# Optimization experiments

Hardware: AMD Instinct MI355X
Metric: run time of the kernel (lower is better)

Reference implementation:

```python
import jax, jax.numpy as jnp
import numpy as np

B, LAT, FRAME, HID, E, GH = 4096, 64, 512, 1024, 8, 128
IN1 = LAT + FRAME      # 576, fc1/gate input
IN2 = LAT + HID        # 1088, fc2/fc3 input
OUT = FRAME            # 512, num_future_frames * frame_size


def setup_inputs() -> dict:
    key = jax.random.key(0)
    ks = jax.random.split(key, 16)
    s = lambda fan_in: 1.0 / np.sqrt(fan_in)
    inp = {
        "z": jax.random.normal(ks[0], (B, LAT), jnp.float32),
        "c": jax.random.normal(ks[1], (B, FRAME), jnp.float32),
        # expert-mixed layers: weight [E, in, out], bias [E, out]
        "w0": jax.random.uniform(ks[2], (E, IN1, HID), jnp.float32, -s(IN1), s(IN1)),
        "b0": jax.random.uniform(ks[3], (E, HID), jnp.float32, -s(IN1), s(IN1)),
        "w1": jax.random.uniform(ks[4], (E, IN2, HID), jnp.float32, -s(IN2), s(IN2)),
        "b1": jax.random.uniform(ks[5], (E, HID), jnp.float32, -s(IN2), s(IN2)),
        "w2": jax.random.uniform(ks[6], (E, IN2, OUT), jnp.float32, -s(IN2), s(IN2)),
        "b2": jax.random.uniform(ks[7], (E, OUT), jnp.float32, -s(IN2), s(IN2)),
        # gate MLP
        "gw1": jax.random.uniform(ks[8], (IN1, GH), jnp.float32, -s(IN1), s(IN1)),
        "gb1": jax.random.uniform(ks[9], (GH,), jnp.float32, -s(IN1), s(IN1)),
        "gw2": jax.random.uniform(ks[10], (GH, GH), jnp.float32, -s(GH), s(GH)),
        "gb2": jax.random.uniform(ks[11], (GH,), jnp.float32, -s(GH), s(GH)),
        "gw3": jax.random.uniform(ks[12], (GH, E), jnp.float32, -s(GH), s(GH)),
        "gb3": jax.random.uniform(ks[13], (E,), jnp.float32, -s(GH), s(GH)),
    }
    return inp


def _mixed_layer(coef, x, w, b):
    # per-expert projection then softmax-weighted mix: same math as
    # baddbmm(coef@b, x, (coef@flat(w)).view(B,in,out)) in the original.
    ye = jnp.einsum('bi,eio->beo', x, w)          # [B, E, out]
    return jnp.einsum('be,beo->bo', coef, ye) + coef @ b


def reference(z, c, w0, b0, w1, b1, w2, b2, gw1, gb1, gw2, gb2, gw3, gb3):
    x0 = jnp.concatenate([z, c], axis=1)           # [B, IN1]
    h = jax.nn.elu(x0 @ gw1 + gb1)
    h = jax.nn.elu(h @ gw2 + gb2)
    coef = jax.nn.softmax(h @ gw3 + gb3, axis=1)   # [B, E]

    out = jax.nn.elu(_mixed_layer(coef, x0, w0, b0))
    out = jax.nn.elu(_mixed_layer(coef, jnp.concatenate([z, out], axis=1), w1, b1))
    out = _mixed_layer(coef, jnp.concatenate([z, out], axis=1), w2, b2)
    return out
```

## Files before the change

kernel.cpp:

```cpp
#include <hip/hip_runtime.h>
#include <cstdint>
#include <cstddef>

#define B_    4096
#define LAT   64
#define FRAME 512
#define HID   1024
#define NE    8
#define GH    128
#define IN1   576
#define IN2   1088

typedef _Float16 half8 __attribute__((ext_vector_type(8)));
typedef float  f32x4  __attribute__((ext_vector_type(4)));

__device__ inline void async16(const void* g, void* l) {
  __builtin_amdgcn_global_load_lds(
      (__attribute__((address_space(1))) void*)(void*)g,
      (__attribute__((address_space(3))) void*)l, 16, 0, 0);
}

__device__ inline float elu(float v) { return v > 0.f ? v : expm1f(v); }

__global__ __launch_bounds__(256) void prep_gatew(
    const float* __restrict__ gw1, const float* __restrict__ gw2,
    _Float16* __restrict__ gw1T, _Float16* __restrict__ gw2T)
{
  __shared__ float t[32][33];
  const int tx = threadIdx.x, ty = threadIdx.y;
  int bx = blockIdx.x;
  const float* in; _Float16* out; int K, N, kt, nt;
  if (bx < 72) { in = gw1; out = gw1T; K = 576; N = 128; kt = bx >> 2; nt = bx & 3; }
  else { bx -= 72; in = gw2; out = gw2T; K = 128; N = 128; kt = bx >> 2; nt = bx & 3; }
  const int k0 = kt * 32, n0 = nt * 32;
  for (int it = 0; it < 4; ++it)
    t[ty + it * 8][tx] = in[(size_t)(k0 + ty + it * 8) * N + n0 + tx];
  __syncthreads();
  for (int it = 0; it < 4; ++it)
    out[(size_t)(n0 + ty + it * 8) * K + k0 + tx] = (_Float16)t[tx][ty + it * 8];
}

__global__ __launch_bounds__(256) void gate_mfma(
    const float* __restrict__ z, const float* __restrict__ c,
    const _Float16* __restrict__ gw1T,
    const _Float16* __restrict__ gw2T,
    const float* __restrict__ gb1, const float* __restrict__ gb2,
    const float* __restrict__ gw3, const float* __restrict__ gb3,
    float* __restrict__ coef)
{
  __shared__ _Float16 h_lds[128][136];
  __shared__ float    h2_lds[128][129];
  __shared__ float    gw3s[128 * 8];
  const int tid = threadIdx.x;
  const int wave = tid >> 6, lane = tid & 63;
  const int quad = lane >> 4, l16 = lane & 15;
  const int r0 = blockIdx.x * 128;

  for (int i = tid; i < 128 * 8; i += 256) gw3s[i] = gw3[i];

  f32x4 acc[2][8];
  #pragma unroll
  for (int mt = 0; mt < 2; ++mt)
    #pragma unroll
    for (int nt = 0; nt < 8; ++nt)
      #pragma unroll
      for (int r = 0; r < 4; ++r) acc[mt][nt][r] = 0.f;

  #pragma unroll 2
  for (int s = 0; s < 18; ++s) {
    const int k0 = s * 32;
    half8 af[2];
    #pragma unroll
    for (int mt = 0; mt < 2; ++mt) {
      const size_t row = r0 + wave * 32 + mt * 16 + l16;
      const float* src = (k0 < LAT) ? z + row * LAT + k0 + quad * 8
                                    : c + row * FRAME + (k0 - LAT) + quad * 8;
      f32x4 lo = *(const f32x4*)src, hi = *(const f32x4*)(src + 4);
      #pragma unroll
      for (int j = 0; j < 4; ++j) { af[mt][j] = (_Float16)lo[j]; af[mt][j + 4] = (_Float16)hi[j]; }
    }
    half8 bfr[8];
    #pragma unroll
    for (int nt = 0; nt < 8; ++nt)
      bfr[nt] = *(const half8*)(gw1T + (size_t)(nt * 16 + l16) * 576 + k0 + quad * 8);
    #pragma unroll
    for (int mt = 0; mt < 2; ++mt)
      #pragma unroll
      for (int nt = 0; nt < 8; ++nt)
        acc[mt][nt] = __builtin_amdgcn_mfma_f32_16x16x32_f16(af[mt], bfr[nt], acc[mt][nt], 0, 0, 0);
  }
  #pragma unroll
  for (int mt = 0; mt < 2; ++mt)
    #pragma unroll
    for (int nt = 0; nt < 8; ++nt)
      #pragma unroll
      for (int r = 0; r < 4; ++r) {
        const int rowl = wave * 32 + mt * 16 + quad * 4 + r;
        const int col = nt * 16 + l16;
        h_lds[rowl][col] = (_Float16)elu(acc[mt][nt][r] + gb1[col]);
      }
  __syncthreads();

  f32x4 acc2[2][8];
  #pragma unroll
  for (int mt = 0; mt < 2; ++mt)
    #pragma unroll
    for (int nt = 0; nt < 8; ++nt)
      #pragma unroll
      for (int r = 0; r < 4; ++r) acc2[mt][nt][r] = 0.f;
  #pragma unroll
  for (int s = 0; s < 4; ++s) {
    const int k0 = s * 32;
    half8 af[2];
    #pragma unroll
    for (int mt = 0; mt < 2; ++mt)
      af[mt] = *(const half8*)&h_lds[wave * 32 + mt * 16 + l16][k0 + quad * 8];
    half8 bfr[8];
    #pragma unroll
    for (int nt = 0; nt < 8; ++nt)
      bfr[nt] = *(const half8*)(gw2T + (size_t)(nt * 16 + l16) * 128 + k0 + quad * 8);
    #pragma unroll
    for (int mt = 0; mt < 2; ++mt)
      #pragma unroll
      for (int nt = 0; nt < 8; ++nt)
        acc2[mt][nt] = __builtin_amdgcn_mfma_f32_16x16x32_f16(af[mt], bfr[nt], acc2[mt][nt], 0, 0, 0);
  }
  #pragma unroll
  for (int mt = 0; mt < 2; ++mt)
    #pragma unroll
    for (int nt = 0; nt < 8; ++nt)
      #pragma unroll
      for (int r = 0; r < 4; ++r) {
        const int rowl = wave * 32 + mt * 16 + quad * 4 + r;
        const int col = nt * 16 + l16;
        h2_lds[rowl][col] = elu(acc2[mt][nt][r] + gb2[col]);
      }
  __syncthreads();

  {
    const int row = tid >> 1, eh = (tid & 1) * 4;
    float l4[4];
    #pragma unroll
    for (int j = 0; j < 4; ++j) l4[j] = gb3[eh + j];
    for (int k = 0; k < 128; ++k) {
      const float hv = h2_lds[row][k];
      #pragma unroll
      for (int j = 0; j < 4; ++j) l4[j] += hv * gw3s[k * 8 + eh + j];
    }
    float m4 = fmaxf(fmaxf(l4[0], l4[1]), fmaxf(l4[2], l4[3]));
    const float M = fmaxf(m4, __shfl_xor(m4, 1));
    float e4[4], s = 0.f;
    #pragma unroll
    for (int j = 0; j < 4; ++j) { e4[j] = expf(l4[j] - M); s += e4[j]; }
    const float inv = 1.f / (s + __shfl_xor(s, 1));
    f32x4 o;
    #pragma unroll
    for (int j = 0; j < 4; ++j) o[j] = e4[j] * inv;
    *(f32x4*)&coef[(size_t)(r0 + row) * NE + eh] = o;
  }
}

__global__ __launch_bounds__(256) void transpose_cast_e(
    const float* __restrict__ in, _Float16* __restrict__ out, int K, int N)
{
  __shared__ float t[64][65];
  const int e = blockIdx.z;
  const int k0 = blockIdx.x * 64, n0 = blockIdx.y * 64;
  const float* ine = in + (size_t)e * K * N;
  _Float16* oute = out + (size_t)e * N * K;
  const int tx = threadIdx.x, ty = threadIdx.y;
  #pragma unroll
  for (int it = 0; it < 16; ++it) {
    const int k = it * 4 + ty;
    t[k][tx] = ine[(size_t)(k0 + k) * N + n0 + tx];
  }
  __syncthreads();
  #pragma unroll
  for (int it = 0; it < 16; ++it) {
    const int n = it * 4 + ty;
    oute[(size_t)(n0 + n) * K + k0 + tx] = (_Float16)t[tx][n];
  }
}

__global__ __launch_bounds__(256) void build_x1(
    const float* __restrict__ z, const float* __restrict__ c,
    _Float16* __restrict__ x1)
{
  int idx = blockIdx.x * 256 + threadIdx.x;
  int b = idx / IN1, j = idx - b * IN1;
  float v = (j < LAT) ? z[(size_t)b * LAT + j] : c[(size_t)b * FRAME + (j - LAT)];
  x1[idx] = (_Float16)v;
}

template<int KDIM, int NOUT, int EG>
__global__ __launch_bounds__(256, 2) void gemm_moe(
    const _Float16* __restrict__ X,
    const _Float16* __restrict__ Wt,
    const float* __restrict__ coef,
    const float* __restrict__ bias,
    float* __restrict__ part)
{
  __shared__ __align__(16) _Float16 As[128 * 64];
  __shared__ __align__(16) _Float16 Bs[2][128 * 64];
  __shared__ float coefS[128 * EG];
  __shared__ float biasS[EG * 128];

  const int tid = threadIdx.x;
  const int wave = tid >> 6, lane = tid & 63;
  const int wm = wave & 1, wn = wave >> 1;
  const int quad = lane >> 4, l16 = lane & 15;
  const int bm0 = blockIdx.x * 128, bn0 = blockIdx.y * 128;
  const int ebase = blockIdx.z * EG;

  for (int i = tid; i < 128 * EG; i += 256)
    coefS[i] = coef[(size_t)(bm0 + i / EG) * NE + ebase + (i % EG)];
  for (int i = tid; i < EG * 128; i += 256)
    biasS[i] = bias[(size_t)(ebase + i / 128) * NOUT + bn0 + (i % 128)];
  __syncthreads();

  _Float16 ch[4][EG];
  #pragma unroll
  for (int mi = 0; mi < 4; ++mi)
    #pragma unroll
    for (int e = 0; e < EG; ++e)
      ch[mi][e] = (_Float16)coefS[(wm * 64 + mi * 16 + l16) * EG + e];

  f32x4 acc[4][4];
  #pragma unroll
  for (int mi = 0; mi < 4; ++mi)
    #pragma unroll
    for (int ni = 0; ni < 4; ++ni)
      #pragma unroll
      for (int r = 0; r < 4; ++r) acc[mi][ni][r] = 0.f;

  const int srow  = wave * 8 + (lane >> 3);
  const int skoff = (((lane & 7) ^ ((lane >> 3) & 7)) * 8);

  constexpr int K0S = KDIM / 64;
  for (int k0i = 0; k0i < K0S; ++k0i) {
    const int k0 = k0i * 64;
    #pragma unroll
    for (int it = 0; it < 4; ++it)
      async16(X + (size_t)(bm0 + it * 32 + srow) * KDIM + k0 + skoff,
              &As[it * 2048 + wave * 512]);
    {
      const size_t eoff = (size_t)ebase * NOUT * KDIM;
      #pragma unroll
      for (int it = 0; it < 4; ++it)
        async16(Wt + eoff + (size_t)(bn0 + it * 32 + srow) * KDIM + k0 + skoff,
                &Bs[0][it * 2048 + wave * 512]);
    }
    __syncthreads();

    half8 af[2][4];
    #pragma unroll
    for (int ks = 0; ks < 2; ++ks)
      #pragma unroll
      for (int mi = 0; mi < 4; ++mi) {
        const int r = wm * 64 + mi * 16 + l16;
        const int g = (ks * 4 + quad) ^ (r & 7);
        af[ks][mi] = *(const half8*)&As[r * 64 + g * 8];
      }

    #pragma unroll
    for (int eo = 0; eo < EG; ++eo) {
      if (eo + 1 < EG) {
        const size_t eoff = (size_t)(ebase + eo + 1) * NOUT * KDIM;
        #pragma unroll
        for (int it = 0; it < 4; ++it)
          async16(Wt + eoff + (size_t)(bn0 + it * 32 + srow) * KDIM + k0 + skoff,
                  &Bs[(eo + 1) & 1][it * 2048 + wave * 512]);
      }
      const _Float16* bsrc = Bs[eo & 1];
      #pragma unroll
      for (int ks = 0; ks < 2; ++ks) {
        half8 bv[4];
        #pragma unroll
        for (int ni = 0; ni < 4; ++ni) {
          const int r = wn * 64 + ni * 16 + l16;
          const int g = (ks * 4 + quad) ^ (r & 7);
          bv[ni] = *(const half8*)&bsrc[r * 64 + g * 8];
        }
        #pragma unroll
        for (int mi = 0; mi < 4; ++mi) {
          const half8 afs = af[ks][mi] * ch[mi][eo];
          #pragma unroll
          for (int ni = 0; ni < 4; ++ni)
            acc[mi][ni] = __builtin_amdgcn_mfma_f32_16x16x32_f16(
                afs, bv[ni], acc[mi][ni], 0, 0, 0);
        }
      }
      __syncthreads();
    }
  }

  float* po = part + (size_t)blockIdx.z * B_ * NOUT;
  #pragma unroll
  for (int mi = 0; mi < 4; ++mi)
    #pragma unroll
    for (int r = 0; r < 4; ++r) {
      const int m_loc = wm * 64 + mi * 16 + quad * 4 + r;
      #pragma unroll
      for (int ni = 0; ni < 4; ++ni) {
        const int n_loc = wn * 64 + ni * 16 + l16;
        float v = acc[mi][ni][r];
        #pragma unroll
        for (int e = 0; e < EG; ++e)
          v += coefS[m_loc * EG + e] * biasS[e * 128 + n_loc];
        po[(size_t)(bm0 + m_loc) * NOUT + bn0 + n_loc] = v;
      }
    }
}

template<int NS>
__global__ __launch_bounds__(256) void expand_x(
    const float* __restrict__ part,
    const float* __restrict__ z,
    _Float16* __restrict__ xn)
{
  int idx = blockIdx.x * 256 + threadIdx.x;
  int b = idx / IN2, j = idx - b * IN2;
  float v;
  if (j < LAT) {
    v = z[(size_t)b * LAT + j];
  } else {
    const int h = j - LAT;
    v = 0.f;
    #pragma unroll
    for (int s = 0; s < NS; ++s)
      v += part[(size_t)s * B_ * HID + (size_t)b * HID + h];
    v = elu(v);
  }
  xn[idx] = (_Float16)v;
}

template<int NS>
__global__ __launch_bounds__(256) void final_out(
    const float* __restrict__ part,
    float* __restrict__ out)
{
  int idx = blockIdx.x * 256 + threadIdx.x;
  float v = 0.f;
  #pragma unroll
  for (int s = 0; s < NS; ++s)
    v += part[(size_t)s * B_ * FRAME + idx];
  out[idx] = v;
}


extern "C" void kernel_launch(void* const* d_in, const int* in_sizes, int n_in,
                              void* d_out, int out_size, void* d_ws, size_t ws_size,
                              hipStream_t stream)
{
  const float* z   = (const float*)d_in[0];
  const float* c   = (const float*)d_in[1];
  const float* w0  = (const float*)d_in[2];
  const float* b0  = (const float*)d_in[3];
  const float* w1  = (const float*)d_in[4];
  const float* b1  = (const float*)d_in[5];
  const float* w2  = (const float*)d_in[6];
  const float* b2  = (const float*)d_in[7];
  const float* gw1 = (const float*)d_in[8];
  const float* gb1 = (const float*)d_in[9];
  const float* gw2 = (const float*)d_in[10];
  const float* gb2 = (const float*)d_in[11];
  const float* gw3 = (const float*)d_in[12];
  const float* gb3 = (const float*)d_in[13];
  float* out = (float*)d_out;
  char* ws = (char*)d_ws;

  float*    coef = (float*)    (ws + 0);
  _Float16* x1   = (_Float16*) (ws + 131072);
  _Float16* x2   = (_Float16*) (ws + 4849664);
  _Float16* x3   = (_Float16*) (ws + 13762560);
  _Float16* Wt0  = (_Float16*) (ws + 22675456);
  _Float16* Wt1  = (_Float16*) (ws + 32112640);
  _Float16* Wt2  = (_Float16*) (ws + 49938432);
  float*    part = (float*)    (ws + 58851328);
  _Float16* gw1T = (_Float16*) (ws + 92405760);
  _Float16* gw2T = (_Float16*) (ws + 92553216);

  prep_gatew<<<88, dim3(32, 8), 0, stream>>>(gw1, gw2, gw1T, gw2T);
  gate_mfma<<<32, 256, 0, stream>>>(z, c, gw1T, gw2T, gb1, gb2, gw3, gb3, coef);
  build_x1<<<(B_ * IN1) / 256, 256, 0, stream>>>(z, c, x1);
  transpose_cast_e<<<dim3(9, 16, NE), dim3(64, 4), 0, stream>>>(w0, Wt0, IN1, HID);
  transpose_cast_e<<<dim3(17, 16, NE), dim3(64, 4), 0, stream>>>(w1, Wt1, IN2, HID);
  transpose_cast_e<<<dim3(17, 8, NE), dim3(64, 4), 0, stream>>>(w2, Wt2, IN2, FRAME);

  gemm_moe<IN1, HID, 4><<<dim3(32, 8, 2), 256, 0, stream>>>(x1, Wt0, coef, b0, part);
  expand_x<2><<<(B_ * IN2) / 256, 256, 0, stream>>>(part, z, x2);

  gemm_moe<IN2, HID, 4><<<dim3(32, 8, 2), 256, 0, stream>>>(x2, Wt1, coef, b1, part);
  expand_x<2><<<(B_ * IN2) / 256, 256, 0, stream>>>(part, z, x3);

  gemm_moe<IN2, FRAME, 2><<<dim3(32, 4, 4), 256, 0, stream>>>(x3, Wt2, coef, b2, part);
  final_out<4><<<(B_ * FRAME) / 256, 256, 0, stream>>>(part, out);
}
```

Measured before the change: 380.9 us.

## Switch MoE GEMM to 32x32 MFMA with double-buffered A, fuse weight prep, vectorize elementwise

The MoE GEMM now uses 32x32x16 MFMA tiles and double-buffers the A tile. The next k-step's A and B loads are issued during the last expert of the current step, so global loads overlap compute. All weight transpose and cast launches are merged into one kernel. The gate kernel uses 64-row blocks for more parallelism, and the elementwise kernels are vectorized to 4 elements per thread. The larger accumulator tiles and extra LDS buffer may raise register and LDS pressure and reduce occupancy.

```diff
diff --git a/kernel.cpp b/kernel.cpp
--- a/kernel.cpp
+++ b/kernel.cpp
@@ -12,7 +12,9 @@
 #define IN2   1088
 
 typedef _Float16 half8 __attribute__((ext_vector_type(8)));
+typedef _Float16 half4 __attribute__((ext_vector_type(4)));
 typedef float  f32x4  __attribute__((ext_vector_type(4)));
+typedef float  f32x16 __attribute__((ext_vector_type(16)));
 
 __device__ inline void async16(const void* g, void* l) {
   __builtin_amdgcn_global_load_lds(
@@ -22,22 +24,51 @@
 
 __device__ inline float elu(float v) { return v > 0.f ? v : expm1f(v); }
 
-__global__ __launch_bounds__(256) void prep_gatew(
-    const float* __restrict__ gw1, const float* __restrict__ gw2,
-    _Float16* __restrict__ gw1T, _Float16* __restrict__ gw2T)
-{
-  __shared__ float t[32][33];
-  const int tx = threadIdx.x, ty = threadIdx.y;
-  int bx = blockIdx.x;
+__global__ __launch_bounds__(256) void prep_weights(
+    const float* __restrict__ w0, const float* __restrict__ w1,
+    const float* __restrict__ w2, const float* __restrict__ gw1,
+    const float* __restrict__ gw2,
+    _Float16* __restrict__ Wt0, _Float16* __restrict__ Wt1,
+    _Float16* __restrict__ Wt2, _Float16* __restrict__ gw1T,
+    _Float16* __restrict__ gw2T)
+{
+  __shared__ float t[64][65];
+  int bid = blockIdx.x;
   const float* in; _Float16* out; int K, N, kt, nt;
-  if (bx < 72) { in = gw1; out = gw1T; K = 576; N = 128; kt = bx >> 2; nt = bx & 3; }
-  else { bx -= 72; in = gw2; out = gw2T; K = 128; N = 128; kt = bx >> 2; nt = bx & 3; }
-  const int k0 = kt * 32, n0 = nt * 32;
-  for (int it = 0; it < 4; ++it)
-    t[ty + it * 8][tx] = in[(size_t)(k0 + ty + it * 8) * N + n0 + tx];
+  if (bid < 1152) {
+    const int e = bid / 144, rem = bid % 144;
+    K = IN1; N = HID; kt = rem / 16; nt = rem % 16;
+    in = w0 + (size_t)e * K * N; out = Wt0 + (size_t)e * N * K;
+  } else if (bid < 3328) {
+    const int i = bid - 1152, e = i / 272, rem = i % 272;
+    K = IN2; N = HID; kt = rem / 16; nt = rem % 16;
+    in = w1 + (size_t)e * K * N; out = Wt1 + (size_t)e * N * K;
+  } else if (bid < 4416) {
+    const int i = bid - 3328, e = i / 136, rem = i % 136;
+    K = IN2; N = FRAME; kt = rem / 8; nt = rem % 8;
+    in = w2 + (size_t)e * K * N; out = Wt2 + (size_t)e * N * K;
+  } else if (bid < 4434) {
+    const int i = bid - 4416;
+    K = IN1; N = GH; kt = i / 2; nt = i % 2;
+    in = gw1; out = gw1T;
+  } else {
+    const int i = bid - 4434;
+    K = GH; N = GH; kt = i / 2; nt = i % 2;
+    in = gw2; out = gw2T;
+  }
+  const int k0 = kt * 64, n0 = nt * 64;
+  const int tx = threadIdx.x & 63, ty = threadIdx.x >> 6;
+  #pragma unroll
+  for (int it = 0; it < 16; ++it) {
+    const int k = it * 4 + ty;
+    t[k][tx] = in[(size_t)(k0 + k) * N + n0 + tx];
+  }
   __syncthreads();
-  for (int it = 0; it < 4; ++it)
-    out[(size_t)(n0 + ty + it * 8) * K + k0 + tx] = (_Float16)t[tx][ty + it * 8];
+  #pragma unroll
+  for (int it = 0; it < 16; ++it) {
+    const int n = it * 4 + ty;
+    out[(size_t)(n0 + n) * K + k0 + tx] = (_Float16)t[tx][n];
+  }
 }
 
 __global__ __launch_bounds__(256) void gate_mfma(
@@ -48,137 +79,97 @@
     const float* __restrict__ gw3, const float* __restrict__ gb3,
     float* __restrict__ coef)
 {
-  __shared__ _Float16 h_lds[128][136];
-  __shared__ float    h2_lds[128][129];
+  __shared__ _Float16 h_lds[64][136];
+  __shared__ float    h2_lds[64][129];
   __shared__ float    gw3s[128 * 8];
   const int tid = threadIdx.x;
   const int wave = tid >> 6, lane = tid & 63;
   const int quad = lane >> 4, l16 = lane & 15;
-  const int r0 = blockIdx.x * 128;
+  const int r0 = blockIdx.x * 64;
 
   for (int i = tid; i < 128 * 8; i += 256) gw3s[i] = gw3[i];
 
-  f32x4 acc[2][8];
-  #pragma unroll
-  for (int mt = 0; mt < 2; ++mt)
-    #pragma unroll
-    for (int nt = 0; nt < 8; ++nt)
-      #pragma unroll
-      for (int r = 0; r < 4; ++r) acc[mt][nt][r] = 0.f;
+  f32x4 acc[8];
+  #pragma unroll
+  for (int nt = 0; nt < 8; ++nt)
+    #pragma unroll
+    for (int r = 0; r < 4; ++r) acc[nt][r] = 0.f;
 
   #pragma unroll 2
   for (int s = 0; s < 18; ++s) {
     const int k0 = s * 32;
-    half8 af[2];
-    #pragma unroll
-    for (int mt = 0; mt < 2; ++mt) {
-      const size_t row = r0 + wave * 32 + mt * 16 + l16;
+    half8 af;
+    {
+      const size_t row = r0 + wave * 16 + l16;
       const float* src = (k0 < LAT) ? z + row * LAT + k0 + quad * 8
                                     : c + row * FRAME + (k0 - LAT) + quad * 8;
       f32x4 lo = *(const f32x4*)src, hi = *(const f32x4*)(src + 4);
       #pragma unroll
-      for (int j = 0; j < 4; ++j) { af[mt][j] = (_Float16)lo[j]; af[mt][j + 4] = (_Float16)hi[j]; }
+      for (int j = 0; j < 4; ++j) { af[j] = (_Float16)lo[j]; af[j + 4] = (_Float16)hi[j]; }
     }
     half8 bfr[8];
     #pragma unroll
     for (int nt = 0; nt < 8; ++nt)
       bfr[nt] = *(const half8*)(gw1T + (size_t)(nt * 16 + l16) * 576 + k0 + quad * 8);
     #pragma unroll
-    for (int mt = 0; mt < 2; ++mt)
-      #pragma unroll
-      for (int nt = 0; nt < 8; ++nt)
-        acc[mt][nt] = __builtin_amdgcn_mfma_f32_16x16x32_f16(af[mt], bfr[nt], acc[mt][nt], 0, 0, 0);
-  }
-  #pragma unroll
-  for (int mt = 0; mt < 2; ++mt)
-    #pragma unroll
     for (int nt = 0; nt < 8; ++nt)
-      #pragma unroll
-      for (int r = 0; r < 4; ++r) {
-        const int rowl = wave * 32 + mt * 16 + quad * 4 + r;
-        const int col = nt * 16 + l16;
-        h_lds[rowl][col] = (_Float16)elu(acc[mt][nt][r] + gb1[col]);
-      }
+      acc[nt] = __builtin_amdgcn_mfma_f32_16x16x32_f16(af, bfr[nt], acc[nt], 0, 0, 0);
+  }
+  #pragma unroll
+  for (int nt = 0; nt < 8; ++nt)
+    #pragma unroll
+    for (int r = 0; r < 4; ++r) {
+      const int rowl = wave * 16 + quad * 4 + r;
+      const int col = nt * 16 + l16;
+      h_lds[rowl][col] = (_Float16)elu(acc[nt][r] + gb1[col]);
+    }
   __syncthreads();
 
-  f32x4 acc2[2][8];
-  #pragma unroll
-  for (int mt = 0; mt < 2; ++mt)
-    #pragma unroll
-    for (int nt = 0; nt < 8; ++nt)
-      #pragma unroll
-      for (int r = 0; r < 4; ++r) acc2[mt][nt][r] = 0.f;
+  f32x4 acc2[8];
+  #pragma unroll
+  for (int nt = 0; nt < 8; ++nt)
+    #pragma unroll
+    for (int r = 0; r < 4; ++r) acc2[nt][r] = 0.f;
   #pragma unroll
   for (int s = 0; s < 4; ++s) {
     const int k0 = s * 32;
-    half8 af[2];
-    #pragma unroll
-    for (int mt = 0; mt < 2; ++mt)
-      af[mt] = *(const half8*)&h_lds[wave * 32 + mt * 16 + l16][k0 + quad * 8];
+    half8 af = *(const half8*)&h_lds[wave * 16 + l16][k0 + quad * 8];
     half8 bfr[8];
     #pragma unroll
     for (int nt = 0; nt < 8; ++nt)
       bfr[nt] = *(const half8*)(gw2T + (size_t)(nt * 16 + l16) * 128 + k0 + quad * 8);
     #pragma unroll
-    for (int mt = 0; mt < 2; ++mt)
-      #pragma unroll
-      for (int nt = 0; nt < 8; ++nt)
-        acc2[mt][nt] = __builtin_amdgcn_mfma_f32_16x16x32_f16(af[mt], bfr[nt], acc2[mt][nt], 0, 0, 0);
-  }
-  #pragma unroll
-  for (int mt = 0; mt < 2; ++mt)
-    #pragma unroll
     for (int nt = 0; nt < 8; ++nt)
-      #pragma unroll
-      for (int r = 0; r < 4; ++r) {
-        const int rowl = wave * 32 + mt * 16 + quad * 4 + r;
-        const int col = nt * 16 + l16;
-        h2_lds[rowl][col] = elu(acc2[mt][nt][r] + gb2[col]);
-      }
+      acc2[nt] = __builtin_amdgcn_mfma_f32_16x16x32_f16(af, bfr[nt], acc2[nt], 0, 0, 0);
+  }
+  #pragma unroll
+  for (int nt = 0; nt < 8; ++nt)
+    #pragma unroll
+    for (int r = 0; r < 4; ++r) {
+      const int rowl = wave * 16 + quad * 4 + r;
+      const int col = nt * 16 + l16;
+      h2_lds[rowl][col] = elu(acc2[nt][r] + gb2[col]);
+    }
   __syncthreads();
 
   {
-    const int row = tid >> 1, eh = (tid & 1) * 4;
-    float l4[4];
-    #pragma unroll
-    for (int j = 0; j < 4; ++j) l4[j] = gb3[eh + j];
+    const int row = tid >> 2, q = tid & 3;
+    float l2v[2] = { gb3[2 * q], gb3[2 * q + 1] };
     for (int k = 0; k < 128; ++k) {
       const float hv = h2_lds[row][k];
-      #pragma unroll
-      for (int j = 0; j < 4; ++j) l4[j] += hv * gw3s[k * 8 + eh + j];
-    }
-    float m4 = fmaxf(fmaxf(l4[0], l4[1]), fmaxf(l4[2], l4[3]));
-    const float M = fmaxf(m4, __shfl_xor(m4, 1));
-    float e4[4], s = 0.f;
-    #pragma unroll
-    for (int j = 0; j < 4; ++j) { e4[j] = expf(l4[j] - M); s += e4[j]; }
-    const float inv = 1.f / (s + __shfl_xor(s, 1));
-    f32x4 o;
-    #pragma unroll
-    for (int j = 0; j < 4; ++j) o[j] = e4[j] * inv;
-    *(f32x4*)&coef[(size_t)(r0 + row) * NE + eh] = o;
-  }
-}
-
-__global__ __launch_bounds__(256) void transpose_cast_e(
-    const float* __restrict__ in, _Float16* __restrict__ out, int K, int N)
-{
-  __shared__ float t[64][65];
-  const int e = blockIdx.z;
-  const int k0 = blockIdx.x * 64, n0 = blockIdx.y * 64;
-  const float* ine = in + (size_t)e * K * N;
-  _Float16* oute = out + (size_t)e * N * K;
-  const int tx = threadIdx.x, ty = threadIdx.y;
-  #pragma unroll
-  for (int it = 0; it < 16; ++it) {
-    const int k = it * 4 + ty;
-    t[k][tx] = ine[(size_t)(k0 + k) * N + n0 + tx];
-  }
-  __syncthreads();
-  #pragma unroll
-  for (int it = 0; it < 16; ++it) {
-    const int n = it * 4 + ty;
-    oute[(size_t)(n0 + n) * K + k0 + tx] = (_Float16)t[tx][n];
+      l2v[0] += hv * gw3s[k * 8 + 2 * q];
+      l2v[1] += hv * gw3s[k * 8 + 2 * q + 1];
+    }
+    float m = fmaxf(l2v[0], l2v[1]);
+    m = fmaxf(m, __shfl_xor(m, 1));
+    m = fmaxf(m, __shfl_xor(m, 2));
+    float e0 = expf(l2v[0] - m), e1 = expf(l2v[1] - m);
+    float s = e0 + e1;
+    s += __shfl_xor(s, 1);
+    s += __shfl_xor(s, 2);
+    const float inv = 1.f / s;
+    float2 o = { e0 * inv, e1 * inv };
+    *(float2*)&coef[(size_t)(r0 + row) * NE + 2 * q] = o;
   }
 }
 
@@ -186,10 +177,14 @@
     const float* __restrict__ z, const float* __restrict__ c,
     _Float16* __restrict__ x1)
 {
-  int idx = blockIdx.x * 256 + threadIdx.x;
-  int b = idx / IN1, j = idx - b * IN1;
-  float v = (j < LAT) ? z[(size_t)b * LAT + j] : c[(size_t)b * FRAME + (j - LAT)];
-  x1[idx] = (_Float16)v;
+  const int idx4 = blockIdx.x * 256 + threadIdx.x;
+  const int b = idx4 / (IN1 / 4), j = (idx4 - b * (IN1 / 4)) * 4;
+  f32x4 v = (j < LAT) ? *(const f32x4*)(z + (size_t)b * LAT + j)
+                      : *(const f32x4*)(c + (size_t)b * FRAME + (j - LAT));
+  half4 o;
+  #pragma unroll
+  for (int q = 0; q < 4; ++q) o[q] = (_Float16)v[q];
+  *(half4*)(x1 + (size_t)b * IN1 + j) = o;
 }
 
 template<int KDIM, int NOUT, int EG>
@@ -200,7 +195,7 @@
     const float* __restrict__ bias,
     float* __restrict__ part)
 {
-  __shared__ __align__(16) _Float16 As[128 * 64];
+  __shared__ __align__(16) _Float16 As[2][128 * 64];
   __shared__ __align__(16) _Float16 Bs[2][128 * 64];
   __shared__ float coefS[128 * EG];
   __shared__ float biasS[EG * 128];
@@ -208,143 +203,148 @@
   const int tid = threadIdx.x;
   const int wave = tid >> 6, lane = tid & 63;
   const int wm = wave & 1, wn = wave >> 1;
-  const int quad = lane >> 4, l16 = lane & 15;
+  const int l32 = lane & 31, khalf = lane >> 5;
   const int bm0 = blockIdx.x * 128, bn0 = blockIdx.y * 128;
   const int ebase = blockIdx.z * EG;
 
   for (int i = tid; i < 128 * EG; i += 256)
     coefS[i] = coef[(size_t)(bm0 + i / EG) * NE + ebase + (i % EG)];
   for (int i = tid; i < EG * 128; i += 256)
-    biasS[i] = bias[(size_t)(ebase + i / 128) * NOUT + bn0 + (i % 128)];
-  __syncthreads();
-
-  _Float16 ch[4][EG];
-  #pragma unroll
-  for (int mi = 0; mi < 4; ++mi)
-    #pragma unroll
-    for (int e = 0; e < EG; ++e)
-      ch[mi][e] = (_Float16)coefS[(wm * 64 + mi * 16 + l16) * EG + e];
-
-  f32x4 acc[4][4];
-  #pragma unroll
-  for (int mi = 0; mi < 4; ++mi)
-    #pragma unroll
-    for (int ni = 0; ni < 4; ++ni)
-      #pragma unroll
-      for (int r = 0; r < 4; ++r) acc[mi][ni][r] = 0.f;
+    biasS[i] = bias[(size_t)(ebase + (i >> 7)) * NOUT + bn0 + (i & 127)];
 
   const int srow  = wave * 8 + (lane >> 3);
   const int skoff = (((lane & 7) ^ ((lane >> 3) & 7)) * 8);
+
+  #define STAGE_A(k0v, buf) \
+    { _Pragma("unroll") \
+      for (int it = 0; it < 4; ++it) \
+        async16(X + (size_t)(bm0 + it * 32 + srow) * KDIM + (k0v) + skoff, \
+                &(buf)[it * 2048 + wave * 512]); }
+  #define STAGE_B(ev, k0v, buf) \
+    { const size_t eoff = (size_t)(ev) * NOUT * KDIM; \
+      _Pragma("unroll") \
+      for (int it = 0; it < 4; ++it) \
+        async16(Wt + eoff + (size_t)(bn0 + it * 32 + srow) * KDIM + (k0v) + skoff, \
+                &(buf)[it * 2048 + wave * 512]); }
+
+  STAGE_A(0, As[0]);
+  STAGE_B(ebase, 0, Bs[0]);
+  __syncthreads();
+
+  _Float16 ch[2][EG];
+  #pragma unroll
+  for (int mi = 0; mi < 2; ++mi)
+    #pragma unroll
+    for (int e = 0; e < EG; ++e)
+      ch[mi][e] = (_Float16)coefS[(wm * 64 + mi * 32 + l32) * EG + e];
+
+  f32x16 acc[2][2];
+  #pragma unroll
+  for (int mi = 0; mi < 2; ++mi)
+    #pragma unroll
+    for (int ni = 0; ni < 2; ++ni)
+      #pragma unroll
+      for (int r = 0; r < 16; ++r) acc[mi][ni][r] = 0.f;
 
   constexpr int K0S = KDIM / 64;
   for (int k0i = 0; k0i < K0S; ++k0i) {
     const int k0 = k0i * 64;
-    #pragma unroll
-    for (int it = 0; it < 4; ++it)
-      async16(X + (size_t)(bm0 + it * 32 + srow) * KDIM + k0 + skoff,
-              &As[it * 2048 + wave * 512]);
-    {
-      const size_t eoff = (size_t)ebase * NOUT * KDIM;
-      #pragma unroll
-      for (int it = 0; it < 4; ++it)
-        async16(Wt + eoff + (size_t)(bn0 + it * 32 + srow) * KDIM + k0 + skoff,
-                &Bs[0][it * 2048 + wave * 512]);
-    }
-    __syncthreads();
-
-    half8 af[2][4];
-    #pragma unroll
-    for (int ks = 0; ks < 2; ++ks)
-      #pragma unroll
-      for (int mi = 0; mi < 4; ++mi) {
-        const int r = wm * 64 + mi * 16 + l16;
-        const int g = (ks * 4 + quad) ^ (r & 7);
-        af[ks][mi] = *(const half8*)&As[r * 64 + g * 8];
+    const int ap = k0i & 1;
+    half8 af[4][2];
+    #pragma unroll
+    for (int ks = 0; ks < 4; ++ks)
+      #pragma unroll
+      for (int mi = 0; mi < 2; ++mi) {
+        const int r = wm * 64 + mi * 32 + l32;
+        const int g = (ks * 2 + khalf) ^ (r & 7);
+        af[ks][mi] = *(const half8*)&As[ap][r * 64 + g * 8];
       }
-
     #pragma unroll
     for (int eo = 0; eo < EG; ++eo) {
       if (eo + 1 < EG) {
-        const size_t eoff = (size_t)(ebase + eo + 1) * NOUT * KDIM;
-        #pragma unroll
-        for (int it = 0; it < 4; ++it)
-          async16(Wt + eoff + (size_t)(bn0 + it * 32 + srow) * KDIM + k0 + skoff,
-                  &Bs[(eo + 1) & 1][it * 2048 + wave * 512]);
+        STAGE_B(ebase + eo + 1, k0, Bs[(eo + 1) & 1]);
+      } else if (k0i + 1 < K0S) {
+        STAGE_A(k0 + 64, As[1 - ap]);
+        STAGE_B(ebase, k0 + 64, Bs[EG & 1]);
       }
       const _Float16* bsrc = Bs[eo & 1];
       #pragma unroll
-      for (int ks = 0; ks < 2; ++ks) {
-        half8 bv[4];
+      for (int ks = 0; ks < 4; ++ks) {
+        half8 bv[2];
         #pragma unroll
-        for (int ni = 0; ni < 4; ++ni) {
-          const int r = wn * 64 + ni * 16 + l16;
-          const int g = (ks * 4 + quad) ^ (r & 7);
+        for (int ni = 0; ni < 2; ++ni) {
+          const int r = wn * 64 + ni * 32 + l32;
+          const int g = (ks * 2 + khalf) ^ (r & 7);
           bv[ni] = *(const half8*)&bsrc[r * 64 + g * 8];
         }
         #pragma unroll
-        for (int mi = 0; mi < 4; ++mi) {
+        for (int mi = 0; mi < 2; ++mi) {
           const half8 afs = af[ks][mi] * ch[mi][eo];
           #pragma unroll
-          for (int ni = 0; ni < 4; ++ni)
-            acc[mi][ni] = __builtin_amdgcn_mfma_f32_16x16x32_f16(
+          for (int ni = 0; ni < 2; ++ni)
+            acc[mi][ni] = __builtin_amdgcn_mfma_f32_32x32x16_f16(
                 afs, bv[ni], acc[mi][ni], 0, 0, 0);
         }
       }
       __syncthreads();
     }
   }
+  #undef STAGE_A
+  #undef STAGE_B
 
   float* po = part + (size_t)blockIdx.z * B_ * NOUT;
   #pragma unroll
-  for (int mi = 0; mi < 4; ++mi)
-    #pragma unroll
-    for (int r = 0; r < 4; ++r) {
-      const int m_loc = wm * 64 + mi * 16 + quad * 4 + r;
-      #pragma unroll
-      for (int ni = 0; ni < 4; ++ni) {
-        const int n_loc = wn * 64 + ni * 16 + l16;
-        float v = acc[mi][ni][r];
+  for (int mi = 0; mi < 2; ++mi)
+    #pragma unroll
+    for (int ni = 0; ni < 2; ++ni)
+      #pragma unroll
+      for (int reg = 0; reg < 16; ++reg) {
+        const int row_l = (reg & 3) + 8 * (reg >> 2) + 4 * khalf;
+        const int m_loc = wm * 64 + mi * 32 + row_l;
+        const int n_loc = wn * 64 + ni * 32 + l32;
+        float v = acc[mi][ni][reg];
         #pragma unroll
         for (int e = 0; e < EG; ++e)
           v += coefS[m_loc * EG + e] * biasS[e * 128 + n_loc];
         po[(size_t)(bm0 + m_loc) * NOUT + bn0 + n_loc] = v;
       }
-    }
-}
-
-template<int NS>
+}
+
 __global__ __launch_bounds__(256) void expand_x(
     const float* __restrict__ part,
     const float* __restrict__ z,
     _Float16* __restrict__ xn)
 {
-  int idx = blockIdx.x * 256 + threadIdx.x;
-  int b = idx / IN2, j = idx - b * IN2;
-  float v;
+  const int idx4 = blockIdx.x * 256 + threadIdx.x;
+  const int b = idx4 / (IN2 / 4), j = (idx4 - b * (IN2 / 4)) * 4;
+  half4 o;
   if (j < LAT) {
-    v = z[(size_t)b * LAT + j];
+    f32x4 v = *(const f32x4*)(z + (size_t)b * LAT + j);
+    #pragma unroll
+    for (int q = 0; q < 4; ++q) o[q] = (_Float16)v[q];
   } else {
     const int h = j - LAT;
-    v = 0.f;
-    #pragma unroll
-    for (int s = 0; s < NS; ++s)
-      v += part[(size_t)s * B_ * HID + (size_t)b * HID + h];
-    v = elu(v);
-  }
-  xn[idx] = (_Float16)v;
-}
-
-template<int NS>
+    f32x4 v0 = *(const f32x4*)(part + (size_t)b * HID + h);
+    f32x4 v1 = *(const f32x4*)(part + (size_t)B_ * HID + (size_t)b * HID + h);
+    #pragma unroll
+    for (int q = 0; q < 4; ++q) o[q] = (_Float16)elu(v0[q] + v1[q]);
+  }
+  *(half4*)(xn + (size_t)b * IN2 + j) = o;
+}
+
 __global__ __launch_bounds__(256) void final_out(
     const float* __restrict__ part,
     float* __restrict__ out)
 {
-  int idx = blockIdx.x * 256 + threadIdx.x;
-  float v = 0.f;
-  #pragma unroll
-  for (int s = 0; s < NS; ++s)
-    v += part[(size_t)s * B_ * FRAME + idx];
-  out[idx] = v;
+  const int idx4 = (blockIdx.x * 256 + threadIdx.x) * 4;
+  f32x4 v = *(const f32x4*)(part + idx4);
+  #pragma unroll
+  for (int s = 1; s < 4; ++s) {
+    f32x4 p = *(const f32x4*)(part + (size_t)s * B_ * FRAME + idx4);
+    #pragma unroll
+    for (int q = 0; q < 4; ++q) v[q] += p[q];
+  }
+  *(f32x4*)(out + idx4) = v;
 }
 
 
@@ -380,19 +380,17 @@
   _Float16* gw1T = (_Float16*) (ws + 92405760);
   _Float16* gw2T = (_Float16*) (ws + 92553216);
 
-  prep_gatew<<<88, dim3(32, 8), 0, stream>>>(gw1, gw2, gw1T, gw2T);
-  gate_mfma<<<32, 256, 0, stream>>>(z, c, gw1T, gw2T, gb1, gb2, gw3, gb3, coef);
-  build_x1<<<(B_ * IN1) / 256, 256, 0, stream>>>(z, c, x1);
-  transpose_cast_e<<<dim3(9, 16, NE), dim3(64, 4), 0, stream>>>(w0, Wt0, IN1, HID);
-  transpose_cast_e<<<dim3(17, 16, NE), dim3(64, 4), 0, stream>>>(w1, Wt1, IN2, HID);
-  transpose_cast_e<<<dim3(17, 8, NE), dim3(64, 4), 0, stream>>>(w2, Wt2, IN2, FRAME);
+  prep_weights<<<4438, 256, 0, stream>>>(w0, w1, w2, gw1, gw2,
+                                         Wt0, Wt1, Wt2, gw1T, gw2T);
+  gate_mfma<<<64, 256, 0, stream>>>(z, c, gw1T, gw2T, gb1, gb2, gw3, gb3, coef);
+  build_x1<<<(B_ * IN1 / 4) / 256, 256, 0, stream>>>(z, c, x1);
 
   gemm_moe<IN1, HID, 4><<<dim3(32, 8, 2), 256, 0, stream>>>(x1, Wt0, coef, b0, part);
-  expand_x<2><<<(B_ * IN2) / 256, 256, 0, stream>>>(part, z, x2);
+  expand_x<<<(B_ * IN2 / 4) / 256, 256, 0, stream>>>(part, z, x2);
 
   gemm_moe<IN2, HID, 4><<<dim3(32, 8, 2), 256, 0, stream>>>(x2, Wt1, coef, b1, part);
-  expand_x<2><<<(B_ * IN2) / 256, 256, 0, stream>>>(part, z, x3);
+  expand_x<<<(B_ * IN2 / 4) / 256, 256, 0, stream>>>(part, z, x3);
 
   gemm_moe<IN2, FRAME, 2><<<dim3(32, 4, 4), 256, 0, stream>>>(x3, Wt2, coef, b2, part);
-  final_out<4><<<(B_ * FRAME) / 256, 256, 0, stream>>>(part, out);
-}
+  final_out<<<(B_ * FRAME / 4) / 256, 256, 0, stream>>>(part, out);
+}
```

After: 356.6 us. -6.4%, faster.
